# Kernel optimization log

Measured on AMD Instinct MI355X. Metric: run time of the kernel, lower is better.

Reference implementation:

```python
import jax, jax.numpy as jnp
import numpy as np

N, D = 8192, 256
E = 65536


def setup_inputs() -> dict:
    key = jax.random.key(0)
    ks = jax.random.split(key, 16)
    s = 1.0 / np.sqrt(D)  # nn.Linear default init scale
    return {
        "x_mean": jax.random.normal(ks[0], (N, D), dtype=jnp.float32),
        "x_var": jax.random.uniform(ks[1], (N, D), dtype=jnp.float32),
        "edge_index": jax.random.randint(ks[2], (2, E), 0, N, dtype=jnp.int64),
        "edge_timestamps": jax.random.uniform(ks[3], (E,), dtype=jnp.float32),
        "Wq": jax.random.uniform(ks[4], (D, D), jnp.float32, -s, s),
        "bq": jax.random.uniform(ks[5], (D,), jnp.float32, -s, s),
        "Wk": jax.random.uniform(ks[6], (D, D), jnp.float32, -s, s),
        "bk": jax.random.uniform(ks[7], (D,), jnp.float32, -s, s),
        "Wv": jax.random.uniform(ks[8], (D, D), jnp.float32, -s, s),
        "bv": jax.random.uniform(ks[9], (D,), jnp.float32, -s, s),
        "Wo": jax.random.uniform(ks[10], (D, D), jnp.float32, -s, s),
        "bo": jax.random.uniform(ks[11], (D,), jnp.float32, -s, s),
        "Wvar": jax.random.uniform(ks[12], (D, D), jnp.float32, -s, s),
        "bvar": jax.random.uniform(ks[13], (D,), jnp.float32, -s, s),
    }


def reference(x_mean, x_var, edge_index, edge_timestamps,
              Wq, bq, Wk, bk, Wv, bv, Wo, bo, Wvar, bvar):
    # edge_index / edge_timestamps are accepted but unused (as in the original forward).
    head_dim = D // 4  # num_heads=4; heads are never split, only used for scale
    scale = head_dim ** -0.5

    q = x_mean @ Wq.T + bq  # [N, D]
    k = x_mean @ Wk.T + bk
    v = x_mean @ Wv.T + bv

    attn = jax.nn.softmax((q @ k.T) * scale, axis=-1)  # [N, N] (dropout: eval mode)

    out_mean = (attn @ v) @ Wo.T + bo  # [N, D]

    v_var = x_var @ Wvar.T + bvar
    out_var = (attn * attn) @ v_var  # squared weights against projected variance
    return out_mean, out_var
```

## Files before the change

### kernel.cpp

```cpp
#include <hip/hip_runtime.h>
#include <hip/hip_bf16.h>
#include <hip/hip_fp16.h>

#define DEV __device__ __forceinline__

typedef __attribute__((ext_vector_type(8))) _Float16 h8;
typedef __attribute__((ext_vector_type(4))) float floatx4;

DEV float bf2f(unsigned short b) { return __uint_as_float(((unsigned)b) << 16); }

DEV void async_ld16(const void* g, void* l) {
  __builtin_amdgcn_global_load_lds(
      (const __attribute__((address_space(1))) unsigned int*)g,
      (__attribute__((address_space(3))) unsigned int*)l, 16, 0, 0);
}

DEV int detect_bf16(const void* x_mean) {
  const unsigned* w = (const unsigned*)x_mean;
  unsigned v = w[threadIdx.x & 63];
  unsigned ex = (v >> 7) & 0xFFu;
  int vote = (ex >= 100u && ex <= 144u) ? 1 : 0;
  unsigned long long b = __ballot(vote);
  return __popcll(b) >= 48 ? 1 : 0;
}

DEV float load_elem(const void* p, int isbf, size_t i) {
  return isbf ? bf2f(((const unsigned short*)p)[i]) : ((const float*)p)[i];
}

DEV void stage8h(const void* src, int isbf, size_t idx, float scale, _Float16* dst) {
  h8 o;
  if (isbf) {
    const unsigned short* s = (const unsigned short*)src + idx;
#pragma unroll
    for (int j = 0; j < 8; ++j) o[j] = (_Float16)(bf2f(s[j]) * scale);
  } else {
    const float* f = (const float*)src + idx;
    float4 a = *(const float4*)f;
    float4 b = *(const float4*)(f + 4);
    o[0] = (_Float16)(a.x * scale); o[1] = (_Float16)(a.y * scale);
    o[2] = (_Float16)(a.z * scale); o[3] = (_Float16)(a.w * scale);
    o[4] = (_Float16)(b.x * scale); o[5] = (_Float16)(b.y * scale);
    o[6] = (_Float16)(b.z * scale); o[7] = (_Float16)(b.w * scale);
  }
  *(h8*)dst = o;
}

struct ProjArgs {
  const void* A[4];
  const void* B[4];
  const void* bias[4];
  _Float16* C[4];
  int fl_tpc[4];
  float scale[4];
  int bias_row[4];
  const void* xdet;
};

__global__ __launch_bounds__(256) void proj_kernel(ProjArgs p) {
  __shared__ __align__(16) char smem[34816];
  _Float16* As = (_Float16*)smem;
  _Float16* Bs = As + 4096;
  _Float16* Ts = (_Float16*)smem;
  int isbf = detect_bf16(p.xdet);
  int z = blockIdx.z;
  size_t i0, j0;
  if (z < 2) { i0 = (size_t)blockIdx.x * 128; j0 = (size_t)blockIdx.y * 128; }
  else       { i0 = (size_t)blockIdx.y * 128; j0 = (size_t)blockIdx.x * 128; }
  const void* A = p.A[z];
  const void* B = p.B[z];
  const void* bias = p.bias[z];
  const float scale = p.scale[z];
  const int bias_row = p.bias_row[z];
  const int tpc = p.fl_tpc[z];
  _Float16* C = p.C[z];
  const int t = threadIdx.x;
  const int lane = t & 63, wave = t >> 6;
  const int wr = wave >> 1, wc = wave & 1;
  const int q = lane >> 4, m = lane & 15;
  floatx4 acc[4][4] = {};
  for (int k0 = 0; k0 < 256; k0 += 32) {
#pragma unroll
    for (int it = 0; it < 2; ++it) {
      int e = it * 2048 + t * 8;
      int row = e >> 5, col = e & 31;
      stage8h(A, isbf, (i0 + row) * (size_t)256 + k0 + col, 1.f, &As[e]);
      stage8h(B, isbf, (j0 + row) * (size_t)256 + k0 + col, 1.f, &Bs[e]);
    }
    __syncthreads();
    h8 af[4], bfr[4];
#pragma unroll
    for (int r = 0; r < 4; ++r)
      af[r] = *(const h8*)&As[(wr * 64 + r * 16 + m) * 32 + q * 8];
#pragma unroll
    for (int c = 0; c < 4; ++c)
      bfr[c] = *(const h8*)&Bs[(wc * 64 + c * 16 + m) * 32 + q * 8];
#pragma unroll
    for (int r = 0; r < 4; ++r)
#pragma unroll
      for (int c = 0; c < 4; ++c)
        acc[r][c] = __builtin_amdgcn_mfma_f32_16x16x32_f16(af[r], bfr[c], acc[r][c], 0, 0, 0);
    __syncthreads();
  }
#pragma unroll
  for (int r = 0; r < 4; ++r)
#pragma unroll
    for (int c = 0; c < 4; ++c) {
      size_t col = j0 + wc * 64 + c * 16 + m;
      float bcol = bias_row ? 0.f : load_elem(bias, isbf, col);
#pragma unroll
      for (int g = 0; g < 4; ++g) {
        size_t row = i0 + wr * 64 + r * 16 + q * 4 + g;
        float val = acc[r][c][g] + bcol;
        if (bias_row) val += load_elem(bias, isbf, row);
        Ts[(wr * 64 + r * 16 + q * 4 + g) * 136 + wc * 64 + c * 16 + m] =
            (_Float16)(val * scale);
      }
    }
  __syncthreads();
  size_t ti0 = i0 >> 4, tj0 = j0 >> 5;
#pragma unroll
  for (int it = 0; it < 8; ++it) {
    int cch = it * 4 + wave;
    int ci = cch >> 2, ck = cch & 3;
    int il = ci * 16 + (lane & 15);
    int jl = ck * 32 + (lane >> 4) * 8;
    h8 v = *(const h8*)&Ts[il * 136 + jl];
    *(h8*)&C[((ti0 + ci) * (size_t)tpc + (tj0 + ck)) * 512 + lane * 8] = v;
  }
}

__global__ __launch_bounds__(256) void qk_exp_kernel(const _Float16* __restrict__ qb,
                                                     const _Float16* __restrict__ kb,
                                                     _Float16* __restrict__ E,
                                                     float* __restrict__ rs) {
  __shared__ __align__(16) char smem[128 * 136 * 2];
  _Float16* As = (_Float16*)smem;
  _Float16* Bs = As + 4096;
  _Float16* Ts = (_Float16*)smem;
  const int t = threadIdx.x;
  const int lane = t & 63, wave = t >> 6;
  const int wr = wave >> 1, wc = wave & 1;
  const int q = lane >> 4, m = lane & 15;
  const size_t bx = blockIdx.x, by = blockIdx.y;
  const size_t i0 = bx * 128;
  floatx4 acc[4][4] = {};
  for (int kt = 0; kt < 8; ++kt) {
#pragma unroll
    for (int it = 0; it < 2; ++it) {
      int c = it * 4 + wave;
      async_ld16(&qb[((bx * 8 + c) * 8 + kt) * 512 + lane * 8], &As[c * 512 + lane * 8]);
      async_ld16(&kb[((by * 8 + c) * 8 + kt) * 512 + lane * 8], &Bs[c * 512 + lane * 8]);
    }
    __syncthreads();
    h8 af[4], bfr[4];
#pragma unroll
    for (int r = 0; r < 4; ++r)
      af[r] = *(const h8*)&As[(wr * 4 + r) * 512 + lane * 8];
#pragma unroll
    for (int c = 0; c < 4; ++c)
      bfr[c] = *(const h8*)&Bs[(wc * 4 + c) * 512 + lane * 8];
#pragma unroll
    for (int r = 0; r < 4; ++r)
#pragma unroll
      for (int c = 0; c < 4; ++c)
        acc[r][c] = __builtin_amdgcn_mfma_f32_16x16x32_f16(af[r], bfr[c], acc[r][c], 0, 0, 0);
    __syncthreads();
  }
#pragma unroll
  for (int r = 0; r < 4; ++r)
#pragma unroll
    for (int c = 0; c < 4; ++c)
#pragma unroll
      for (int g = 0; g < 4; ++g)
        acc[r][c][g] = __expf(fminf(acc[r][c][g], 8.f)) * 0.015625f;
#pragma unroll
  for (int r = 0; r < 4; ++r)
#pragma unroll
    for (int g = 0; g < 4; ++g) {
      float part = acc[r][0][g] + acc[r][1][g] + acc[r][2][g] + acc[r][3][g];
      part += __shfl_xor(part, 1);
      part += __shfl_xor(part, 2);
      part += __shfl_xor(part, 4);
      part += __shfl_xor(part, 8);
      if (m == 0)
        unsafeAtomicAdd(&rs[i0 + wr * 64 + r * 16 + q * 4 + g], part);
    }
#pragma unroll
  for (int r = 0; r < 4; ++r)
#pragma unroll
    for (int c = 0; c < 4; ++c)
#pragma unroll
      for (int g = 0; g < 4; ++g)
        Ts[(wr * 64 + r * 16 + q * 4 + g) * 136 + wc * 64 + c * 16 + m] =
            (_Float16)acc[r][c][g];
  __syncthreads();
#pragma unroll
  for (int it = 0; it < 8; ++it) {
    int cch = it * 4 + wave;
    int ci = cch >> 2, ck = cch & 3;
    int il = ci * 16 + (lane & 15);
    int jl = ck * 32 + (lane >> 4) * 8;
    h8 v = *(const h8*)&Ts[il * 136 + jl];
    *(h8*)&E[((bx * 8 + ci) * 256 + by * 4 + ck) * 512 + lane * 8] = v;
  }
}

__global__ __launch_bounds__(256) void zero_rs_kernel(float* __restrict__ rs) {
  rs[blockIdx.x * 256 + threadIdx.x] = 0.f;
}
__global__ __launch_bounds__(256) void zero_acc_kernel(float* __restrict__ a,
                                                       float* __restrict__ b) {
  size_t i = ((size_t)blockIdx.x * 256 + threadIdx.x) * 4;
  float4 z = {0.f, 0.f, 0.f, 0.f};
  *(float4*)(a + i) = z;
  *(float4*)(b + i) = z;
}

__global__ __launch_bounds__(256, 4) void av_fused(const _Float16* __restrict__ E,
                                                   const _Float16* __restrict__ vT,
                                                   const _Float16* __restrict__ vvT,
                                                   const float* __restrict__ rs,
                                                   float* __restrict__ otm,
                                                   float* __restrict__ otv) {
  __shared__ __align__(16) _Float16 As[4 * 512];
  __shared__ __align__(16) _Float16 B1s[8 * 512];
  __shared__ __align__(16) _Float16 B2s[8 * 512];
  const int t = threadIdx.x;
  const int lane = t & 63, wave = t >> 6;
  const int wr = wave >> 1, wc = wave & 1;
  const int q = lane >> 4, m = lane & 15;
  const size_t bx = blockIdx.x, by = blockIdx.y;
  const int kt0 = (blockIdx.z == 0) ? 0 : 86 + (blockIdx.z - 1) * 85;
  const int ktn = (blockIdx.z == 0) ? 86 : 85;
  size_t aoff = ((bx * 4 + (size_t)wave) * 256 + (size_t)kt0) * 512 + lane * 8;
  size_t boff0 = ((by * 8 + (size_t)wave) * 256 + (size_t)kt0) * 512 + lane * 8;
  size_t boff1 = ((by * 8 + (size_t)wave + 4) * 256 + (size_t)kt0) * 512 + lane * 8;
  floatx4 accm[2][4] = {}, accv[2][4] = {};
  for (int kk = 0; kk < ktn; ++kk) {
    async_ld16(&E[aoff], &As[wave * 512 + lane * 8]);
    async_ld16(&vT[boff0], &B1s[wave * 512 + lane * 8]);
    async_ld16(&vT[boff1], &B1s[(wave + 4) * 512 + lane * 8]);
    async_ld16(&vvT[boff0], &B2s[wave * 512 + lane * 8]);
    async_ld16(&vvT[boff1], &B2s[(wave + 4) * 512 + lane * 8]);
    __syncthreads();
    h8 a[2], a2[2], b1[4], b2[4];
#pragma unroll
    for (int r = 0; r < 2; ++r) {
      a[r] = *(const h8*)&As[(wr * 2 + r) * 512 + lane * 8];
      a2[r] = a[r] * a[r];
    }
#pragma unroll
    for (int c = 0; c < 4; ++c) {
      b1[c] = *(const h8*)&B1s[(wc * 4 + c) * 512 + lane * 8];
      b2[c] = *(const h8*)&B2s[(wc * 4 + c) * 512 + lane * 8];
    }
#pragma unroll
    for (int r = 0; r < 2; ++r)
#pragma unroll
      for (int c = 0; c < 4; ++c) {
        accm[r][c] = __builtin_amdgcn_mfma_f32_16x16x32_f16(a[r], b1[c], accm[r][c], 0, 0, 0);
        accv[r][c] = __builtin_amdgcn_mfma_f32_16x16x32_f16(a2[r], b2[c], accv[r][c], 0, 0, 0);
      }
    __syncthreads();
    aoff += 512; boff0 += 512; boff1 += 512;
  }
#pragma unroll
  for (int r = 0; r < 2; ++r)
#pragma unroll
    for (int g = 0; g < 4; ++g) {
      size_t row = bx * 64 + wr * 32 + r * 16 + q * 4 + g;
      float inv = 1.f / rs[row];
      float inv2 = inv * inv;
#pragma unroll
      for (int c = 0; c < 4; ++c) {
        size_t col = by * 128 + wc * 64 + c * 16 + m;
        unsafeAtomicAdd(&otm[row * 256 + col], accm[r][c][g] * inv);
        unsafeAtomicAdd(&otv[row * 256 + col], accv[r][c][g] * inv2);
      }
    }
}

__global__ __launch_bounds__(256) void final_kernel(const float* __restrict__ ot,
                                                    const void* Wo, const void* bo,
                                                    const void* xdet,
                                                    float* __restrict__ Cm) {
  __shared__ __align__(16) _Float16 As[64 * 32];
  __shared__ __align__(16) _Float16 Bs[128 * 32];
  int isbf = detect_bf16(xdet);
  const int t = threadIdx.x;
  const int lane = t & 63, wave = t >> 6;
  const int wr = wave >> 1, wc = wave & 1;
  const int q = lane >> 4, m = lane & 15;
  const size_t i0 = (size_t)blockIdx.x * 64, j0 = (size_t)blockIdx.y * 128;
  floatx4 acc[2][4] = {};
  for (int k0 = 0; k0 < 256; k0 += 32) {
    {
      int e = t * 8;
      int row = e >> 5, col = e & 31;
      stage8h(ot, 0, (i0 + row) * (size_t)256 + k0 + col, 1.f, &As[e]);
    }
#pragma unroll
    for (int it = 0; it < 2; ++it) {
      int e = it * 2048 + t * 8;
      int row = e >> 5, col = e & 31;
      stage8h(Wo, isbf, (j0 + row) * (size_t)256 + k0 + col, 1.f, &Bs[e]);
    }
    __syncthreads();
    h8 af[2], bfr[4];
#pragma unroll
    for (int r = 0; r < 2; ++r)
      af[r] = *(const h8*)&As[(wr * 32 + r * 16 + m) * 32 + q * 8];
#pragma unroll
    for (int c = 0; c < 4; ++c)
      bfr[c] = *(const h8*)&Bs[(wc * 64 + c * 16 + m) * 32 + q * 8];
#pragma unroll
    for (int r = 0; r < 2; ++r)
#pragma unroll
      for (int c = 0; c < 4; ++c)
        acc[r][c] = __builtin_amdgcn_mfma_f32_16x16x32_f16(af[r], bfr[c], acc[r][c], 0, 0, 0);
    __syncthreads();
  }
#pragma unroll
  for (int r = 0; r < 2; ++r)
#pragma unroll
    for (int c = 0; c < 4; ++c) {
      size_t col = j0 + wc * 64 + c * 16 + m;
      float bcol = load_elem(bo, isbf, col);
#pragma unroll
      for (int g = 0; g < 4; ++g) {
        size_t row = i0 + wr * 32 + r * 16 + q * 4 + g;
        Cm[row * 256 + col] = acc[r][c][g] + bcol;
      }
    }
}

extern "C" void kernel_launch(void* const* d_in, const int* in_sizes, int n_in,
                              void* d_out, int out_size, void* d_ws, size_t ws_size,
                              hipStream_t stream) {
  const void* x_mean = d_in[0];
  const void* x_var  = d_in[1];
  const void* Wq   = d_in[4];
  const void* bq   = d_in[5];
  const void* Wk   = d_in[6];
  const void* bk   = d_in[7];
  const void* Wv   = d_in[8];
  const void* bv   = d_in[9];
  const void* Wo   = d_in[10];
  const void* bo   = d_in[11];
  const void* Wvar = d_in[12];
  const void* bvar = d_in[13];
  float* out = (float*)d_out;

  const size_t NE_S = 67108864;
  const size_t NE_P = 2097152;
  if (ws_size < (NE_S + 5 * NE_P) * 2) return;
  _Float16* w   = (_Float16*)d_ws;
  _Float16* S   = w;
  _Float16* qb  = w + NE_S;
  _Float16* kb  = qb + NE_P;
  _Float16* vT  = kb + NE_P;
  _Float16* vvT = vT + NE_P;
  float* rs     = (float*)(vvT + NE_P);
  float* ot_f32 = (float*)qb;

  ProjArgs p;
  p.A[0] = x_mean; p.B[0] = Wq;     p.bias[0] = bq;   p.C[0] = qb;  p.fl_tpc[0] = 8;   p.scale[0] = 0.125f; p.bias_row[0] = 0;
  p.A[1] = x_mean; p.B[1] = Wk;     p.bias[1] = bk;   p.C[1] = kb;  p.fl_tpc[1] = 8;   p.scale[1] = 1.f;    p.bias_row[1] = 0;
  p.A[2] = Wv;     p.B[2] = x_mean; p.bias[2] = bv;   p.C[2] = vT;  p.fl_tpc[2] = 256; p.scale[2] = 1.f;    p.bias_row[2] = 1;
  p.A[3] = Wvar;   p.B[3] = x_var;  p.bias[3] = bvar; p.C[3] = vvT; p.fl_tpc[3] = 256; p.scale[3] = 1.f;    p.bias_row[3] = 1;
  p.xdet = x_mean;

  zero_rs_kernel<<<dim3(32), 256, 0, stream>>>(rs);
  proj_kernel<<<dim3(64, 2, 4), 256, 0, stream>>>(p);
  qk_exp_kernel<<<dim3(64, 64), 256, 0, stream>>>(qb, kb, S, rs);
  zero_acc_kernel<<<dim3(2048), 256, 0, stream>>>(ot_f32, out + NE_P);
  av_fused<<<dim3(128, 2, 3), 256, 0, stream>>>(S, vT, vvT, rs, ot_f32, out + NE_P);
  final_kernel<<<dim3(128, 2), 256, 0, stream>>>(ot_f32, Wo, bo, x_mean, out);
}
```

Baseline: 322.4 us.

## Fold Wo into value projection and drop final output GEMM

Precomputes M = Wo·Wv and c = Wo·bv in a small prep kernel, so the value projection directly yields Wo-projected values and attention output accumulates straight into the final output, seeded with bo. This removes the final GEMM kernel and the intermediate f32 buffer, and merges the zeroing kernels into one seed kernel. av_fused now loads the A fragments directly from global memory into registers instead of staging them through LDS, and splits K into 4 chunks of 64 instead of 3. The extra split adds more atomics, and rounding M to fp16 can slightly change precision.

```diff
diff --git a/kernel.cpp b/kernel.cpp
--- a/kernel.cpp
+++ b/kernel.cpp
@@ -28,22 +28,102 @@
   return isbf ? bf2f(((const unsigned short*)p)[i]) : ((const float*)p)[i];
 }
 
-DEV void stage8h(const void* src, int isbf, size_t idx, float scale, _Float16* dst) {
+DEV void stage8h(const void* src, int isbf, size_t idx, _Float16* dst) {
   h8 o;
   if (isbf) {
     const unsigned short* s = (const unsigned short*)src + idx;
 #pragma unroll
-    for (int j = 0; j < 8; ++j) o[j] = (_Float16)(bf2f(s[j]) * scale);
+    for (int j = 0; j < 8; ++j) o[j] = (_Float16)bf2f(s[j]);
   } else {
     const float* f = (const float*)src + idx;
     float4 a = *(const float4*)f;
     float4 b = *(const float4*)(f + 4);
-    o[0] = (_Float16)(a.x * scale); o[1] = (_Float16)(a.y * scale);
-    o[2] = (_Float16)(a.z * scale); o[3] = (_Float16)(a.w * scale);
-    o[4] = (_Float16)(b.x * scale); o[5] = (_Float16)(b.y * scale);
-    o[6] = (_Float16)(b.z * scale); o[7] = (_Float16)(b.w * scale);
+    o[0] = (_Float16)a.x; o[1] = (_Float16)a.y;
+    o[2] = (_Float16)a.z; o[3] = (_Float16)a.w;
+    o[4] = (_Float16)b.x; o[5] = (_Float16)b.y;
+    o[6] = (_Float16)b.z; o[7] = (_Float16)b.w;
   }
   *(h8*)dst = o;
+}
+
+DEV void stage8t(const void* src, int isbf, size_t base, size_t stride, _Float16* dst) {
+  h8 o;
+#pragma unroll
+  for (int j = 0; j < 8; ++j) o[j] = (_Float16)load_elem(src, isbf, base + (size_t)j * stride);
+  *(h8*)dst = o;
+}
+
+__global__ __launch_bounds__(256) void zero_seed(float* __restrict__ om,
+                                                 float* __restrict__ ov,
+                                                 float* __restrict__ rs,
+                                                 const void* bo, const void* xdet) {
+  int isbf = detect_bf16(xdet);
+  size_t idx = (size_t)blockIdx.x * 256 + threadIdx.x;
+  size_t i = idx * 4;
+  if (idx < 524288) {
+    int c0 = (int)(i & 255);
+    float4 v = {load_elem(bo, isbf, c0), load_elem(bo, isbf, c0 + 1),
+                load_elem(bo, isbf, c0 + 2), load_elem(bo, isbf, c0 + 3)};
+    *(float4*)(om + i) = v;
+  } else {
+    float4 z = {0.f, 0.f, 0.f, 0.f};
+    *(float4*)(ov + (i - 2097152)) = z;
+  }
+  if (blockIdx.x < 32) rs[blockIdx.x * 256 + threadIdx.x] = 0.f;
+}
+
+__global__ __launch_bounds__(256) void prep_kernel(const void* Wo, const void* Wv,
+                                                   const void* bv, const void* xdet,
+                                                   float* __restrict__ M,
+                                                   float* __restrict__ c) {
+  __shared__ __align__(16) _Float16 As[4096];
+  __shared__ __align__(16) _Float16 Bs[4096];
+  int isbf = detect_bf16(xdet);
+  const int t = threadIdx.x;
+  const int lane = t & 63, wave = t >> 6;
+  const int wr = wave >> 1, wc = wave & 1;
+  const int q = lane >> 4, m = lane & 15;
+  const size_t i0 = (size_t)blockIdx.x * 128, j0 = (size_t)blockIdx.y * 128;
+  if (blockIdx.x == 0 && blockIdx.y == 0) {
+    float s = 0.f;
+    for (int j = 0; j < 256; ++j) s += load_elem(Wo, isbf, (size_t)t * 256 + j) * load_elem(bv, isbf, j);
+    c[t] = s;
+  }
+  floatx4 acc[4][4] = {};
+  for (int k0 = 0; k0 < 256; k0 += 32) {
+#pragma unroll
+    for (int it = 0; it < 2; ++it) {
+      int e = it * 2048 + t * 8;
+      int row = e >> 5, col = e & 31;
+      stage8h(Wo, isbf, (i0 + row) * (size_t)256 + k0 + col, &As[e]);
+      stage8t(Wv, isbf, (size_t)(k0 + col) * 256 + (j0 + row), 256, &Bs[e]);
+    }
+    __syncthreads();
+    h8 af[4], bfr[4];
+#pragma unroll
+    for (int r = 0; r < 4; ++r)
+      af[r] = *(const h8*)&As[(wr * 64 + r * 16 + m) * 32 + q * 8];
+#pragma unroll
+    for (int cc = 0; cc < 4; ++cc)
+      bfr[cc] = *(const h8*)&Bs[(wc * 64 + cc * 16 + m) * 32 + q * 8];
+#pragma unroll
+    for (int r = 0; r < 4; ++r)
+#pragma unroll
+      for (int cc = 0; cc < 4; ++cc)
+        acc[r][cc] = __builtin_amdgcn_mfma_f32_16x16x32_f16(af[r], bfr[cc], acc[r][cc], 0, 0, 0);
+    __syncthreads();
+  }
+#pragma unroll
+  for (int r = 0; r < 4; ++r)
+#pragma unroll
+    for (int cc = 0; cc < 4; ++cc) {
+      size_t col = j0 + wc * 64 + cc * 16 + m;
+#pragma unroll
+      for (int g = 0; g < 4; ++g) {
+        size_t row = i0 + wr * 64 + r * 16 + q * 4 + g;
+        M[row * 256 + col] = acc[r][cc][g];
+      }
+    }
 }
 
 struct ProjArgs {
@@ -54,6 +134,8 @@
   int fl_tpc[4];
   float scale[4];
   int bias_row[4];
+  int a_f32[4];
+  int bias_f32[4];
   const void* xdet;
 };
 
@@ -73,6 +155,8 @@
   const float scale = p.scale[z];
   const int bias_row = p.bias_row[z];
   const int tpc = p.fl_tpc[z];
+  const int a_bf = p.a_f32[z] ? 0 : isbf;
+  const int bias_bf = p.bias_f32[z] ? 0 : isbf;
   _Float16* C = p.C[z];
   const int t = threadIdx.x;
   const int lane = t & 63, wave = t >> 6;
@@ -84,8 +168,8 @@
     for (int it = 0; it < 2; ++it) {
       int e = it * 2048 + t * 8;
       int row = e >> 5, col = e & 31;
-      stage8h(A, isbf, (i0 + row) * (size_t)256 + k0 + col, 1.f, &As[e]);
-      stage8h(B, isbf, (j0 + row) * (size_t)256 + k0 + col, 1.f, &Bs[e]);
+      stage8h(A, a_bf, (i0 + row) * (size_t)256 + k0 + col, &As[e]);
+      stage8h(B, isbf, (j0 + row) * (size_t)256 + k0 + col, &Bs[e]);
     }
     __syncthreads();
     h8 af[4], bfr[4];
@@ -107,12 +191,12 @@
 #pragma unroll
     for (int c = 0; c < 4; ++c) {
       size_t col = j0 + wc * 64 + c * 16 + m;
-      float bcol = bias_row ? 0.f : load_elem(bias, isbf, col);
+      float bcol = bias_row ? 0.f : load_elem(bias, bias_bf, col);
 #pragma unroll
       for (int g = 0; g < 4; ++g) {
         size_t row = i0 + wr * 64 + r * 16 + q * 4 + g;
         float val = acc[r][c][g] + bcol;
-        if (bias_row) val += load_elem(bias, isbf, row);
+        if (bias_row) val += load_elem(bias, bias_bf, row);
         Ts[(wr * 64 + r * 16 + q * 4 + g) * 136 + wc * 64 + c * 16 + m] =
             (_Float16)(val * scale);
       }
@@ -206,24 +290,12 @@
   }
 }
 
-__global__ __launch_bounds__(256) void zero_rs_kernel(float* __restrict__ rs) {
-  rs[blockIdx.x * 256 + threadIdx.x] = 0.f;
-}
-__global__ __launch_bounds__(256) void zero_acc_kernel(float* __restrict__ a,
-                                                       float* __restrict__ b) {
-  size_t i = ((size_t)blockIdx.x * 256 + threadIdx.x) * 4;
-  float4 z = {0.f, 0.f, 0.f, 0.f};
-  *(float4*)(a + i) = z;
-  *(float4*)(b + i) = z;
-}
-
 __global__ __launch_bounds__(256, 4) void av_fused(const _Float16* __restrict__ E,
-                                                   const _Float16* __restrict__ vT,
+                                                   const _Float16* __restrict__ uT,
                                                    const _Float16* __restrict__ vvT,
                                                    const float* __restrict__ rs,
-                                                   float* __restrict__ otm,
-                                                   float* __restrict__ otv) {
-  __shared__ __align__(16) _Float16 As[4 * 512];
+                                                   float* __restrict__ om,
+                                                   float* __restrict__ ov) {
   __shared__ __align__(16) _Float16 B1s[8 * 512];
   __shared__ __align__(16) _Float16 B2s[8 * 512];
   const int t = threadIdx.x;
@@ -231,39 +303,32 @@
   const int wr = wave >> 1, wc = wave & 1;
   const int q = lane >> 4, m = lane & 15;
   const size_t bx = blockIdx.x, by = blockIdx.y;
-  const int kt0 = (blockIdx.z == 0) ? 0 : 86 + (blockIdx.z - 1) * 85;
-  const int ktn = (blockIdx.z == 0) ? 86 : 85;
-  size_t aoff = ((bx * 4 + (size_t)wave) * 256 + (size_t)kt0) * 512 + lane * 8;
+  const int kt0 = blockIdx.z * 64;
   size_t boff0 = ((by * 8 + (size_t)wave) * 256 + (size_t)kt0) * 512 + lane * 8;
   size_t boff1 = ((by * 8 + (size_t)wave + 4) * 256 + (size_t)kt0) * 512 + lane * 8;
+  const _Float16* ap0 = E + ((bx * 4 + (size_t)(wr * 2 + 0)) * 256 + (size_t)kt0) * 512 + lane * 8;
+  const _Float16* ap1 = E + ((bx * 4 + (size_t)(wr * 2 + 1)) * 256 + (size_t)kt0) * 512 + lane * 8;
   floatx4 accm[2][4] = {}, accv[2][4] = {};
-  for (int kk = 0; kk < ktn; ++kk) {
-    async_ld16(&E[aoff], &As[wave * 512 + lane * 8]);
-    async_ld16(&vT[boff0], &B1s[wave * 512 + lane * 8]);
-    async_ld16(&vT[boff1], &B1s[(wave + 4) * 512 + lane * 8]);
+  for (int kk = 0; kk < 64; ++kk) {
+    async_ld16(&uT[boff0], &B1s[wave * 512 + lane * 8]);
+    async_ld16(&uT[boff1], &B1s[(wave + 4) * 512 + lane * 8]);
     async_ld16(&vvT[boff0], &B2s[wave * 512 + lane * 8]);
     async_ld16(&vvT[boff1], &B2s[(wave + 4) * 512 + lane * 8]);
-    __syncthreads();
-    h8 a[2], a2[2], b1[4], b2[4];
-#pragma unroll
-    for (int r = 0; r < 2; ++r) {
-      a[r] = *(const h8*)&As[(wr * 2 + r) * 512 + lane * 8];
-      a2[r] = a[r] * a[r];
-    }
+    h8 a0 = *(const h8*)ap0;
+    h8 a1 = *(const h8*)ap1;
+    __syncthreads();
+    h8 a0q = a0 * a0, a1q = a1 * a1;
 #pragma unroll
     for (int c = 0; c < 4; ++c) {
-      b1[c] = *(const h8*)&B1s[(wc * 4 + c) * 512 + lane * 8];
-      b2[c] = *(const h8*)&B2s[(wc * 4 + c) * 512 + lane * 8];
-    }
-#pragma unroll
-    for (int r = 0; r < 2; ++r)
-#pragma unroll
-      for (int c = 0; c < 4; ++c) {
-        accm[r][c] = __builtin_amdgcn_mfma_f32_16x16x32_f16(a[r], b1[c], accm[r][c], 0, 0, 0);
-        accv[r][c] = __builtin_amdgcn_mfma_f32_16x16x32_f16(a2[r], b2[c], accv[r][c], 0, 0, 0);
-      }
-    __syncthreads();
-    aoff += 512; boff0 += 512; boff1 += 512;
+      h8 b1 = *(const h8*)&B1s[(wc * 4 + c) * 512 + lane * 8];
+      h8 b2 = *(const h8*)&B2s[(wc * 4 + c) * 512 + lane * 8];
+      accm[0][c] = __builtin_amdgcn_mfma_f32_16x16x32_f16(a0, b1, accm[0][c], 0, 0, 0);
+      accm[1][c] = __builtin_amdgcn_mfma_f32_16x16x32_f16(a1, b1, accm[1][c], 0, 0, 0);
+      accv[0][c] = __builtin_amdgcn_mfma_f32_16x16x32_f16(a0q, b2, accv[0][c], 0, 0, 0);
+      accv[1][c] = __builtin_amdgcn_mfma_f32_16x16x32_f16(a1q, b2, accv[1][c], 0, 0, 0);
+    }
+    __syncthreads();
+    ap0 += 512; ap1 += 512; boff0 += 512; boff1 += 512;
   }
 #pragma unroll
   for (int r = 0; r < 2; ++r)
@@ -275,62 +340,8 @@
 #pragma unroll
       for (int c = 0; c < 4; ++c) {
         size_t col = by * 128 + wc * 64 + c * 16 + m;
-        unsafeAtomicAdd(&otm[row * 256 + col], accm[r][c][g] * inv);
-        unsafeAtomicAdd(&otv[row * 256 + col], accv[r][c][g] * inv2);
-      }
-    }
-}
-
-__global__ __launch_bounds__(256) void final_kernel(const float* __restrict__ ot,
-                                                    const void* Wo, const void* bo,
-                                                    const void* xdet,
-                                                    float* __restrict__ Cm) {
-  __shared__ __align__(16) _Float16 As[64 * 32];
-  __shared__ __align__(16) _Float16 Bs[128 * 32];
-  int isbf = detect_bf16(xdet);
-  const int t = threadIdx.x;
-  const int lane = t & 63, wave = t >> 6;
-  const int wr = wave >> 1, wc = wave & 1;
-  const int q = lane >> 4, m = lane & 15;
-  const size_t i0 = (size_t)blockIdx.x * 64, j0 = (size_t)blockIdx.y * 128;
-  floatx4 acc[2][4] = {};
-  for (int k0 = 0; k0 < 256; k0 += 32) {
-    {
-      int e = t * 8;
-      int row = e >> 5, col = e & 31;
-      stage8h(ot, 0, (i0 + row) * (size_t)256 + k0 + col, 1.f, &As[e]);
-    }
-#pragma unroll
-    for (int it = 0; it < 2; ++it) {
-      int e = it * 2048 + t * 8;
-      int row = e >> 5, col = e & 31;
-      stage8h(Wo, isbf, (j0 + row) * (size_t)256 + k0 + col, 1.f, &Bs[e]);
-    }
-    __syncthreads();
-    h8 af[2], bfr[4];
-#pragma unroll
-    for (int r = 0; r < 2; ++r)
-      af[r] = *(const h8*)&As[(wr * 32 + r * 16 + m) * 32 + q * 8];
-#pragma unroll
-    for (int c = 0; c < 4; ++c)
-      bfr[c] = *(const h8*)&Bs[(wc * 64 + c * 16 + m) * 32 + q * 8];
-#pragma unroll
-    for (int r = 0; r < 2; ++r)
-#pragma unroll
-      for (int c = 0; c < 4; ++c)
-        acc[r][c] = __builtin_amdgcn_mfma_f32_16x16x32_f16(af[r], bfr[c], acc[r][c], 0, 0, 0);
-    __syncthreads();
-  }
-#pragma unroll
-  for (int r = 0; r < 2; ++r)
-#pragma unroll
-    for (int c = 0; c < 4; ++c) {
-      size_t col = j0 + wc * 64 + c * 16 + m;
-      float bcol = load_elem(bo, isbf, col);
-#pragma unroll
-      for (int g = 0; g < 4; ++g) {
-        size_t row = i0 + wr * 32 + r * 16 + q * 4 + g;
-        Cm[row * 256 + col] = acc[r][c][g] + bcol;
+        unsafeAtomicAdd(&om[row * 256 + col], accm[r][c][g] * inv);
+        unsafeAtomicAdd(&ov[row * 256 + col], accv[r][c][g] * inv2);
       }
     }
 }
@@ -359,22 +370,22 @@
   _Float16* S   = w;
   _Float16* qb  = w + NE_S;
   _Float16* kb  = qb + NE_P;
-  _Float16* vT  = kb + NE_P;
-  _Float16* vvT = vT + NE_P;
+  _Float16* uT  = kb + NE_P;
+  _Float16* vvT = uT + NE_P;
   float* rs     = (float*)(vvT + NE_P);
-  float* ot_f32 = (float*)qb;
+  float* M      = rs + 8192;
+  float* c      = M + 65536;
 
   ProjArgs p;
-  p.A[0] = x_mean; p.B[0] = Wq;     p.bias[0] = bq;   p.C[0] = qb;  p.fl_tpc[0] = 8;   p.scale[0] = 0.125f; p.bias_row[0] = 0;
-  p.A[1] = x_mean; p.B[1] = Wk;     p.bias[1] = bk;   p.C[1] = kb;  p.fl_tpc[1] = 8;   p.scale[1] = 1.f;    p.bias_row[1] = 0;
-  p.A[2] = Wv;     p.B[2] = x_mean; p.bias[2] = bv;   p.C[2] = vT;  p.fl_tpc[2] = 256; p.scale[2] = 1.f;    p.bias_row[2] = 1;
-  p.A[3] = Wvar;   p.B[3] = x_var;  p.bias[3] = bvar; p.C[3] = vvT; p.fl_tpc[3] = 256; p.scale[3] = 1.f;    p.bias_row[3] = 1;
+  p.A[0] = x_mean; p.B[0] = Wq;     p.bias[0] = bq;   p.C[0] = qb;  p.fl_tpc[0] = 8;   p.scale[0] = 0.125f; p.bias_row[0] = 0; p.a_f32[0] = 0; p.bias_f32[0] = 0;
+  p.A[1] = x_mean; p.B[1] = Wk;     p.bias[1] = bk;   p.C[1] = kb;  p.fl_tpc[1] = 8;   p.scale[1] = 1.f;    p.bias_row[1] = 0; p.a_f32[1] = 0; p.bias_f32[1] = 0;
+  p.A[2] = M;      p.B[2] = x_mean; p.bias[2] = c;    p.C[2] = uT;  p.fl_tpc[2] = 256; p.scale[2] = 1.f;    p.bias_row[2] = 1; p.a_f32[2] = 1; p.bias_f32[2] = 1;
+  p.A[3] = Wvar;   p.B[3] = x_var;  p.bias[3] = bvar; p.C[3] = vvT; p.fl_tpc[3] = 256; p.scale[3] = 1.f;    p.bias_row[3] = 1; p.a_f32[3] = 0; p.bias_f32[3] = 0;
   p.xdet = x_mean;
 
-  zero_rs_kernel<<<dim3(32), 256, 0, stream>>>(rs);
+  zero_seed<<<dim3(4096), 256, 0, stream>>>(out, out + NE_P, rs, bo, x_mean);
+  prep_kernel<<<dim3(2, 2), 256, 0, stream>>>(Wo, Wv, bv, x_mean, M, c);
   proj_kernel<<<dim3(64, 2, 4), 256, 0, stream>>>(p);
   qk_exp_kernel<<<dim3(64, 64), 256, 0, stream>>>(qb, kb, S, rs);
-  zero_acc_kernel<<<dim3(2048), 256, 0, stream>>>(ot_f32, out + NE_P);
-  av_fused<<<dim3(128, 2, 3), 256, 0, stream>>>(S, vT, vvT, rs, ot_f32, out + NE_P);
-  final_kernel<<<dim3(128, 2), 256, 0, stream>>>(ot_f32, Wo, bo, x_mean, out);
-}
+  av_fused<<<dim3(128, 2, 4), 256, 0, stream>>>(S, uT, vvT, rs, out, out + NE_P);
+}
```

New measurement: 356.9 us. 10.7% more time.
